# Optimization experiments

Measured on AMD Instinct MI355X. Metric: run time of the kernel, lower is better.

The kernel has to match this reference:

```python
import jax, jax.numpy as jnp
import numpy as np

ALPHA_SCALE = 9.9
EPS_LN = 1e-5
EPS_NORM = 1e-12


def _ln(x, g, b):
    m = x.mean(axis=-1, keepdims=True)
    v = ((x - m) ** 2).mean(axis=-1, keepdims=True)
    return (x - m) / jnp.sqrt(v + EPS_LN) * g + b


def setup_inputs() -> dict:
    key = jax.random.key(0)
    ks = jax.random.split(key, 8)
    B, D, U = 32, 4096, 64
    return {
        "stimulus": jax.random.normal(ks[0], (B, D), jnp.float32),
        "prev_act": jax.random.normal(ks[1], (B, D), jnp.float32),
        "W_heb": jax.random.normal(ks[2], (D, D), jnp.float32),
        "W_rec": jax.random.normal(ks[3], (D, D), jnp.float32),
        "decay": jax.random.uniform(ks[4], (D,), jnp.float32),
        "ln_rec_g": jnp.ones((D,), jnp.float32),
        "ln_rec_b": jnp.zeros((D,), jnp.float32),
        "fc1_w": jax.random.normal(ks[5], (D, 512), jnp.float32) * 0.02,
        "fc1_b": jnp.zeros((512,), jnp.float32),
        "ln1_g": jnp.ones((512,), jnp.float32),
        "ln1_b": jnp.zeros((512,), jnp.float32),
        "fc2_w": jax.random.normal(ks[6], (512, 256), jnp.float32) * 0.05,
        "fc2_b": jnp.zeros((256,), jnp.float32),
        "ln2_g": jnp.ones((256,), jnp.float32),
        "ln2_b": jnp.zeros((256,), jnp.float32),
        "fc3_w": jax.random.normal(ks[7], (256, U), jnp.float32) * 0.05,
        "fc3_b": jnp.zeros((U,), jnp.float32),
        "lno_g": jnp.ones((U,), jnp.float32),
        "lno_b": jnp.zeros((U,), jnp.float32),
    }


def reference(stimulus, prev_act, W_heb, W_rec, decay, ln_rec_g, ln_rec_b,
              fc1_w, fc1_b, ln1_g, ln1_b, fc2_w, fc2_b, ln2_g, ln2_b,
              fc3_w, fc3_b, lno_g, lno_b):
    D = W_heb.shape[0]
    U = fc3_b.shape[0]
    # recurrent path
    rec_out = jax.nn.relu(prev_act @ W_rec)           # [B, D]
    rec_norm = _ln(rec_out, ln_rec_g, ln_rec_b)
    # stimulus path
    stim_out = jax.nn.relu(stimulus @ W_heb)          # [B, D]
    final = stim_out + rec_norm                       # [B, D]
    # neuromodulator MLP -> dopamine (mean over batch)
    h = jax.nn.relu(_ln(final @ fc1_w + fc1_b, ln1_g, ln1_b))
    h = jax.nn.relu(_ln(h @ fc2_w + fc2_b, ln2_g, ln2_b))
    dop = jnp.tanh(_ln(h @ fc3_w + fc3_b, lno_g, lno_b)).mean(axis=0)  # [U]
    alpha = jnp.repeat(dop, D // U) * ALPHA_SCALE                      # [D]
    # Hebbian updates: batched outer products accumulated = GEMM
    heb_upd = jnp.einsum('bi,bj->ij', stimulus, stim_out)   # [D, D]
    rec_upd = jnp.einsum('bi,bj->ij', prev_act, rec_out)    # [D, D]
    W1 = W_heb + heb_upd * alpha[None, :]
    W2 = W_rec + rec_upd * alpha[None, :]
    # decay: W - diag(decay) @ W == (1 - decay) row-scale
    W1 = W1 * (1.0 - decay)[:, None]
    W2 = W2 * (1.0 - decay)[:, None]
    # row-wise L2 normalize (F.normalize p=2 dim=1)
    W1 = W1 / jnp.maximum(jnp.linalg.norm(W1, axis=1, keepdims=True), EPS_NORM)
    W2 = W2 / jnp.maximum(jnp.linalg.norm(W2, axis=1, keepdims=True), EPS_NORM)
    # [B+2D, D]: final_output followed by the two updated weight buffers
    return jnp.concatenate([final, W1, W2], axis=0)
```

## Files before the change

### kernel.cpp

```cpp
#include <hip/hip_runtime.h>
#include <stdint.h>

typedef unsigned short ushort_t;
typedef float f32x4 __attribute__((ext_vector_type(4)));
typedef short s16x8 __attribute__((ext_vector_type(8)));

#define B_  32
#define D_  4096
#define H1_ 512
#define H2_ 256
#define U_  64

#define KS_   16
#define KCH_  256
#define NT_   128
#define APAD  264
#define WPAD  70

__device__ __forceinline__ float bf2f(ushort_t u) {
    return __uint_as_float(((uint32_t)u) << 16);
}
__device__ __forceinline__ ushort_t f2bfu(float f) {
    uint32_t x = __float_as_uint(f);
    return (ushort_t)((x + 0x7fffu + ((x >> 16) & 1u)) >> 16);
}
__device__ __forceinline__ uint32_t pk2bf(float a, float b) {
    return ((uint32_t)f2bfu(a)) | (((uint32_t)f2bfu(b)) << 16);
}

__global__ __launch_bounds__(256, 4) void k_gemm_mfma(
    const float* __restrict__ stim, const float* __restrict__ prev,
    const float* __restrict__ Wheb, const float* __restrict__ Wrec,
    float* __restrict__ Psum, int ns)
{
    __shared__ ushort_t Al[32 * APAD];
    __shared__ ushort_t Wt[NT_ * WPAD];

    int bx = blockIdx.x;
    int gemm  = bx >> 9;
    int rem   = bx & 511;
    int nblk  = rem >> 4;
    int chunk = rem & 15;
    const float* A = gemm ? prev : stim;
    const float* W = gemm ? Wrec : Wheb;
    int k0c = chunk * KCH_;
    int n0  = nblk * NT_;
    int tid = threadIdx.x, lane = tid & 63, wave = tid >> 6;
    int col = lane & 15, quad = lane >> 4;

#pragma unroll
    for (int p = 0; p < 8; p++) {
        int idx = p * 256 + tid;
        int b   = idx >> 6;
        int k4  = (idx & 63) * 4;
        float4 v = *(const float4*)(A + (size_t)b * D_ + k0c + k4);
        uint2 w; w.x = pk2bf(v.x, v.y); w.y = pk2bf(v.z, v.w);
        *(uint2*)&Al[b * APAD + k4] = w;
    }

    f32x4 acc[2][2];
#pragma unroll
    for (int mt = 0; mt < 2; mt++)
#pragma unroll
        for (int nt = 0; nt < 2; nt++)
            acc[mt][nt] = (f32x4){0.f, 0.f, 0.f, 0.f};

    int m = tid & 31;
    int g = tid >> 5;

    for (int ks = 0; ks < 4; ks++) {
        __syncthreads();
        const float* Wb = W + (size_t)(k0c + ks * 64) * D_ + n0 + m * 4;
#pragma unroll
        for (int i = 0; i < 4; i++) {
            int kp = g + 8 * i;
            const float* p0 = Wb + (size_t)(2 * kp) * D_;
            float4 r0 = *(const float4*)p0;
            float4 r1 = *(const float4*)(p0 + D_);
            *(uint32_t*)&Wt[(m * 4 + 0) * WPAD + 2 * kp] = pk2bf(r0.x, r1.x);
            *(uint32_t*)&Wt[(m * 4 + 1) * WPAD + 2 * kp] = pk2bf(r0.y, r1.y);
            *(uint32_t*)&Wt[(m * 4 + 2) * WPAD + 2 * kp] = pk2bf(r0.z, r1.z);
            *(uint32_t*)&Wt[(m * 4 + 3) * WPAD + 2 * kp] = pk2bf(r0.w, r1.w);
        }
        __syncthreads();

#pragma unroll
        for (int kq = 0; kq < 2; kq++) {
            int kb = ks * 64 + kq * 32 + quad * 8;
            int kw = kq * 32 + quad * 8;
            s16x8 af[2], bf[2];
            af[0] = *(const s16x8*)&Al[col * APAD + kb];
            af[1] = *(const s16x8*)&Al[(col + 16) * APAD + kb];
#pragma unroll
            for (int nt = 0; nt < 2; nt++)
                bf[nt] = *(const s16x8*)&Wt[(wave * 32 + nt * 16 + col) * WPAD + kw];
#pragma unroll
            for (int mt = 0; mt < 2; mt++)
#pragma unroll
                for (int nt = 0; nt < 2; nt++)
                    acc[mt][nt] = __builtin_amdgcn_mfma_f32_16x16x32_bf16(
                        af[mt], bf[nt], acc[mt][nt], 0, 0, 0);
        }
    }

    int slice = chunk % ns;
    float* P = Psum + ((size_t)slice * 2 + gemm) * 32 * D_;
    if (ns == 16) {
#pragma unroll
        for (int mt = 0; mt < 2; mt++)
#pragma unroll
            for (int nt = 0; nt < 2; nt++)
#pragma unroll
                for (int r = 0; r < 4; r++) {
                    int b = mt * 16 + quad * 4 + r;
                    int n = n0 + wave * 32 + nt * 16 + col;
                    P[(size_t)b * D_ + n] = acc[mt][nt][r];
                }
    } else {
#pragma unroll
        for (int mt = 0; mt < 2; mt++)
#pragma unroll
            for (int nt = 0; nt < 2; nt++)
#pragma unroll
                for (int r = 0; r < 4; r++) {
                    int b = mt * 16 + quad * 4 + r;
                    int n = n0 + wave * 32 + nt * 16 + col;
                    atomicAdd(&P[(size_t)b * D_ + n], acc[mt][nt][r]);
                }
    }
}

__global__ __launch_bounds__(256) void k_reduce(
    const float* __restrict__ Psum,
    const float* __restrict__ stim, const float* __restrict__ prev,
    float* __restrict__ P_relu, ushort_t* __restrict__ Tbuf, int ns)
{
    int idx = blockIdx.x * 256 + threadIdx.x;
    int gemm = idx >> 17;
    int r    = idx & 131071;
    int b    = r >> 12;
    int d    = r & 4095;
    float s = 0.f;
    for (int sl = 0; sl < ns; sl++)
        s += Psum[((size_t)sl * 2 + gemm) * 131072 + r];
    s = fmaxf(s, 0.f);
    P_relu[idx] = s;
    Tbuf[(2 + gemm) * 131072 + d * 32 + b] = f2bfu(s);
    Tbuf[gemm * 131072 + d * 32 + b] = f2bfu((gemm ? prev : stim)[r]);
}

__global__ __launch_bounds__(256) void k_final_ln(
    const float* __restrict__ P_relu,
    const float* __restrict__ g, const float* __restrict__ be,
    float* __restrict__ dout, float* __restrict__ finalf32)
{
    __shared__ float red[256], red2[256];
    int b = blockIdx.x, tid = threadIdx.x;
    const float* rec = P_relu + 131072 + b * D_;
    const float* stm = P_relu + b * D_;

    float s = 0.f, s2 = 0.f;
    for (int d = tid; d < D_; d += 256) { float x = rec[d]; s += x; s2 += x * x; }
    red[tid] = s; red2[tid] = s2; __syncthreads();
    for (int st = 128; st > 0; st >>= 1) {
        if (tid < st) { red[tid] += red[tid + st]; red2[tid] += red2[tid + st]; }
        __syncthreads();
    }
    float m = red[0] * (1.f / D_);
    float v = red2[0] * (1.f / D_) - m * m;
    float rstd = rsqrtf(v + 1e-5f);

    for (int d = tid; d < D_; d += 256) {
        float fn = stm[d] + (rec[d] - m) * rstd * g[d] + be[d];
        finalf32[b * D_ + d] = fn;
        dout[b * D_ + d] = fn;
    }
}

__global__ __launch_bounds__(256) void k_fc1(
    const float* __restrict__ finalf32, const float* __restrict__ fc1w,
    float* __restrict__ z1p)
{
    int kc = blockIdx.x;
    int t  = threadIdx.x;
    int k0 = kc * 64;
    const float2* W2 = (const float2*)fc1w;

    float a0[32], a1[32];
#pragma unroll
    for (int b = 0; b < 32; b++) { a0[b] = 0.f; a1[b] = 0.f; }

    for (int k = k0; k < k0 + 64; k++) {
        float2 wv = W2[k * (H1_ / 2) + t];
#pragma unroll
        for (int b = 0; b < 32; b++) {
            float a = finalf32[b * D_ + k];
            a0[b] = fmaf(a, wv.x, a0[b]);
            a1[b] = fmaf(a, wv.y, a1[b]);
        }
    }
    float* P = z1p + (size_t)kc * 32 * H1_;
#pragma unroll
    for (int b = 0; b < 32; b++) {
        P[b * H1_ + 2 * t]     = a0[b];
        P[b * H1_ + 2 * t + 1] = a1[b];
    }
}

__global__ __launch_bounds__(256) void k_tail(
    const float* __restrict__ z1p,
    const float* __restrict__ fc1b,
    const float* __restrict__ ln1g, const float* __restrict__ ln1b,
    const float* __restrict__ fc2w, const float* __restrict__ fc2b,
    const float* __restrict__ ln2g, const float* __restrict__ ln2b,
    const float* __restrict__ fc3w, const float* __restrict__ fc3b,
    const float* __restrict__ lnog, const float* __restrict__ lnob,
    float* __restrict__ tanhout)
{
    __shared__ float sm[512];
    __shared__ float red[256], red2[256];
    __shared__ float h2s[256];
    int b = blockIdx.x, tid = threadIdx.x;

    for (int j = tid; j < H1_; j += 256) {
        float s = fc1b[j];
        for (int c = 0; c < 64; c++)
            s += z1p[((size_t)c * 32 + b) * H1_ + j];
        sm[j] = s;
    }
    __syncthreads();

    float s = 0.f, s2 = 0.f;
    for (int j = tid; j < H1_; j += 256) { float x = sm[j]; s += x; s2 += x * x; }
    red[tid] = s; red2[tid] = s2; __syncthreads();
    for (int st = 128; st > 0; st >>= 1) {
        if (tid < st) { red[tid] += red[tid + st]; red2[tid] += red2[tid + st]; }
        __syncthreads();
    }
    float m = red[0] * (1.f / H1_);
    float v = red2[0] * (1.f / H1_) - m * m;
    float rstd = rsqrtf(v + 1e-5f);
    __syncthreads();
    for (int j = tid; j < H1_; j += 256) {
        float h = (sm[j] - m) * rstd * ln1g[j] + ln1b[j];
        sm[j] = fmaxf(h, 0.f);
    }
    __syncthreads();

    float acc = fc2b[tid];
    for (int k = 0; k < H1_; k++)
        acc = fmaf(sm[k], fc2w[k * H2_ + tid], acc);
    red[tid] = acc; red2[tid] = acc * acc; __syncthreads();
    for (int st = 128; st > 0; st >>= 1) {
        if (tid < st) { red[tid] += red[tid + st]; red2[tid] += red2[tid + st]; }
        __syncthreads();
    }
    float m2 = red[0] * (1.f / H2_);
    float v2 = red2[0] * (1.f / H2_) - m2 * m2;
    float rstd2 = rsqrtf(v2 + 1e-5f);
    float h2 = fmaxf((acc - m2) * rstd2 * ln2g[tid] + ln2b[tid], 0.f);
    __syncthreads();
    h2s[tid] = h2; __syncthreads();

    int j  = tid & 63;
    int ks = tid >> 6;
    float p = 0.f;
    for (int kk = 0; kk < 64; kk++) {
        int k = ks * 64 + kk;
        p = fmaf(h2s[k], fc3w[k * U_ + j], p);
    }
    red[tid] = p; __syncthreads();
    if (tid < 64) {
        float x = red[tid] + red[tid + 64] + red[tid + 128] + red[tid + 192]
                + fc3b[tid];
        float ss = x, qq = x * x;
#pragma unroll
        for (int off = 32; off; off >>= 1) {
            ss += __shfl_xor(ss, off, 64);
            qq += __shfl_xor(qq, off, 64);
        }
        float m3 = ss * (1.f / U_);
        float v3 = qq * (1.f / U_) - m3 * m3;
        float to = tanhf((x - m3) * rsqrtf(v3 + 1e-5f) * lnog[tid] + lnob[tid]);
        tanhout[b * U_ + tid] = to;
    }
}

__global__ __launch_bounds__(512, 2) void k_update(
    const float* __restrict__ Wheb, const float* __restrict__ Wrec,
    const float* __restrict__ decay, const float* __restrict__ tanhout,
    const ushort_t* __restrict__ Tbuf, float* __restrict__ dout)
{
    __shared__ float ssl[8][16];
    int bx   = blockIdx.x;
    int mat  = bx >> 8;
    int i0   = (bx & 255) * 16;
    int tid  = threadIdx.x;
    int wave = tid >> 6, lane = tid & 63;
    int col  = lane & 15, quad = lane >> 4;

    float al = 0.f;
#pragma unroll
    for (int b = 0; b < 32; b++) al += tanhout[b * U_ + lane];
    al *= (9.9f / 32.f);

    const ushort_t* Sp = Tbuf + mat * 131072;
    const ushort_t* Op = Tbuf + (2 + mat) * 131072;
    const float*    Wp = mat ? Wrec : Wheb;

    s16x8 bfr = *(const s16x8*)&Sp[(i0 + col) * 32 + quad * 8];

    float dc = 1.f - decay[i0 + col];

    uint32_t vc[32][2];
    float ss = 0.f;

#pragma unroll
    for (int t = 0; t < 32; t++) {
        int tile = t * 8 + wave;
        int j0   = tile * 16;
        float av = __shfl(al, tile >> 2, 64);
        s16x8 af = *(const s16x8*)&Op[(j0 + col) * 32 + quad * 8];
        f32x4 u = (f32x4){0.f, 0.f, 0.f, 0.f};
        u = __builtin_amdgcn_mfma_f32_16x16x32_bf16(af, bfr, u, 0, 0, 0);
        const float4 w4 = *(const float4*)(Wp + (size_t)(i0 + col) * D_
                                           + j0 + quad * 4);
        float v0 = fmaf(av, u[0], w4.x) * dc;
        float v1 = fmaf(av, u[1], w4.y) * dc;
        float v2 = fmaf(av, u[2], w4.z) * dc;
        float v3 = fmaf(av, u[3], w4.w) * dc;
        ss = fmaf(v0, v0, ss);
        ss = fmaf(v1, v1, ss);
        ss = fmaf(v2, v2, ss);
        ss = fmaf(v3, v3, ss);
        vc[t][0] = pk2bf(v0, v1);
        vc[t][1] = pk2bf(v2, v3);
    }

    ss += __shfl_xor(ss, 16, 64);
    ss += __shfl_xor(ss, 32, 64);
    if (quad == 0) ssl[wave][col] = ss;
    __syncthreads();
    float st = 0.f;
#pragma unroll
    for (int w = 0; w < 8; w++) st += ssl[w][col];
    float ri = 1.f / fmaxf(sqrtf(st), 1e-12f);

    float* O = dout + (size_t)(32 + mat * D_ + i0 + col) * D_;
#pragma unroll
    for (int t = 0; t < 32; t++) {
        int j0 = (t * 8 + wave) * 16 + quad * 4;
        float4 o;
        o.x = __uint_as_float(vc[t][0] << 16)         * ri;
        o.y = __uint_as_float(vc[t][0] & 0xffff0000u) * ri;
        o.z = __uint_as_float(vc[t][1] << 16)         * ri;
        o.w = __uint_as_float(vc[t][1] & 0xffff0000u) * ri;
        *(float4*)(O + j0) = o;
    }
}

extern "C" void kernel_launch(void* const* d_in, const int* in_sizes, int n_in,
                              void* d_out, int out_size, void* d_ws, size_t ws_size,
                              hipStream_t stream)
{
    const float* stim = (const float*)d_in[0];
    const float* prev = (const float*)d_in[1];
    const float* Wheb = (const float*)d_in[2];
    const float* Wrec = (const float*)d_in[3];
    const float* decay= (const float*)d_in[4];
    const float* lnrg = (const float*)d_in[5];
    const float* lnrb = (const float*)d_in[6];
    const float* fc1w = (const float*)d_in[7];
    const float* fc1b = (const float*)d_in[8];
    const float* ln1g = (const float*)d_in[9];
    const float* ln1b = (const float*)d_in[10];
    const float* fc2w = (const float*)d_in[11];
    const float* fc2b = (const float*)d_in[12];
    const float* ln2g = (const float*)d_in[13];
    const float* ln2b = (const float*)d_in[14];
    const float* fc3w = (const float*)d_in[15];
    const float* fc3b = (const float*)d_in[16];
    const float* lnog = (const float*)d_in[17];
    const float* lnob = (const float*)d_in[18];

    const size_t FIXED = 1048576u + 1048576u + 524288u + 4194304u + 8192u;
    int ns = 16;
    if (ws_size < FIXED + 16u * 1048576u) {
        size_t avail = (ws_size > FIXED) ? (ws_size - FIXED) / 1048576u : 1u;
        ns = (int)avail;
        if (ns < 1) ns = 1;
        if (ns > 16) ns = 16;
    }

    char* ws = (char*)d_ws;
    float*    P_sum   = (float*)(ws + 0);
    char*     rest    = ws + (size_t)ns * 1048576u;
    float*    P_relu  = (float*)(rest + 0);
    ushort_t* P_tbuf  = (ushort_t*)(rest + 1048576);
    float*    P_final = (float*)(rest + 2097152);
    float*    P_z1p   = (float*)(rest + 2621440);
    float*    P_tanh  = (float*)(rest + 6815744);

    float* out = (float*)d_out;

    if (ns < 16)
        hipMemsetAsync(P_sum, 0, (size_t)ns * 1048576u, stream);

    k_gemm_mfma<<<1024, 256, 0, stream>>>(stim, prev, Wheb, Wrec, P_sum, ns);
    k_reduce   <<<1024, 256, 0, stream>>>(P_sum, stim, prev, P_relu, P_tbuf, ns);
    k_final_ln <<<32,   256, 0, stream>>>(P_relu, lnrg, lnrb, out, P_final);
    k_fc1      <<<64,   256, 0, stream>>>(P_final, fc1w, P_z1p);
    k_tail     <<<32,   256, 0, stream>>>(P_z1p, fc1b, ln1g, ln1b, fc2w, fc2b,
                                          ln2g, ln2b, fc3w, fc3b, lnog, lnob, P_tanh);
    k_update   <<<512,  512, 0, stream>>>(Wheb, Wrec, decay, P_tanh, P_tbuf, out);
}
```

Before: 403.2 us.

## Prefetch GEMM weight tiles, coalesce reduce transposes, vectorize LN, drop duplicate final buffer

The GEMM kernel now loads the next 64-row W chunk into registers while the current chunk is packed to LDS, so global load latency overlaps with the MFMA work. The reduce kernel processes float4 slices and transposes through shared memory, which turns the scattered 2-byte transposed writes into coalesced 8-byte writes. The final LayerNorm uses float4 loads and stores and no longer writes a separate fp32 copy; fc1 reads the output buffer directly. These changes cost extra registers in the GEMM and an LDS barrier in the reduce kernel.

```diff
diff --git a/kernel.cpp b/kernel.cpp
--- a/kernel.cpp
+++ b/kernel.cpp
@@ -68,19 +68,35 @@
     int m = tid & 31;
     int g = tid >> 5;
 
+    float4 pr0[4], pr1[4];
+    {
+        const float* Wb = W + (size_t)k0c * D_ + n0 + m * 4;
+#pragma unroll
+        for (int i = 0; i < 4; i++) {
+            int kp = g + 8 * i;
+            pr0[i] = *(const float4*)(Wb + (size_t)(2 * kp) * D_);
+            pr1[i] = *(const float4*)(Wb + (size_t)(2 * kp) * D_ + D_);
+        }
+    }
+
     for (int ks = 0; ks < 4; ks++) {
         __syncthreads();
-        const float* Wb = W + (size_t)(k0c + ks * 64) * D_ + n0 + m * 4;
 #pragma unroll
         for (int i = 0; i < 4; i++) {
             int kp = g + 8 * i;
-            const float* p0 = Wb + (size_t)(2 * kp) * D_;
-            float4 r0 = *(const float4*)p0;
-            float4 r1 = *(const float4*)(p0 + D_);
-            *(uint32_t*)&Wt[(m * 4 + 0) * WPAD + 2 * kp] = pk2bf(r0.x, r1.x);
-            *(uint32_t*)&Wt[(m * 4 + 1) * WPAD + 2 * kp] = pk2bf(r0.y, r1.y);
-            *(uint32_t*)&Wt[(m * 4 + 2) * WPAD + 2 * kp] = pk2bf(r0.z, r1.z);
-            *(uint32_t*)&Wt[(m * 4 + 3) * WPAD + 2 * kp] = pk2bf(r0.w, r1.w);
+            *(uint32_t*)&Wt[(m * 4 + 0) * WPAD + 2 * kp] = pk2bf(pr0[i].x, pr1[i].x);
+            *(uint32_t*)&Wt[(m * 4 + 1) * WPAD + 2 * kp] = pk2bf(pr0[i].y, pr1[i].y);
+            *(uint32_t*)&Wt[(m * 4 + 2) * WPAD + 2 * kp] = pk2bf(pr0[i].z, pr1[i].z);
+            *(uint32_t*)&Wt[(m * 4 + 3) * WPAD + 2 * kp] = pk2bf(pr0[i].w, pr1[i].w);
+        }
+        if (ks < 3) {
+            const float* Wb = W + (size_t)(k0c + (ks + 1) * 64) * D_ + n0 + m * 4;
+#pragma unroll
+            for (int i = 0; i < 4; i++) {
+                int kp = g + 8 * i;
+                pr0[i] = *(const float4*)(Wb + (size_t)(2 * kp) * D_);
+                pr1[i] = *(const float4*)(Wb + (size_t)(2 * kp) * D_ + D_);
+            }
         }
         __syncthreads();
 
@@ -135,24 +151,49 @@
     const float* __restrict__ stim, const float* __restrict__ prev,
     float* __restrict__ P_relu, ushort_t* __restrict__ Tbuf, int ns)
 {
-    int idx = blockIdx.x * 256 + threadIdx.x;
-    int gemm = idx >> 17;
-    int r    = idx & 131071;
-    int b    = r >> 12;
-    int d    = r & 4095;
-    float s = 0.f;
-    for (int sl = 0; sl < ns; sl++)
-        s += Psum[((size_t)sl * 2 + gemm) * 131072 + r];
-    s = fmaxf(s, 0.f);
-    P_relu[idx] = s;
-    Tbuf[(2 + gemm) * 131072 + d * 32 + b] = f2bfu(s);
-    Tbuf[gemm * 131072 + d * 32 + b] = f2bfu((gemm ? prev : stim)[r]);
+    __shared__ ushort_t T0[32][33];
+    __shared__ ushort_t T1[32][33];
+    int bx   = blockIdx.x;
+    int gemm = bx >> 7;
+    int d0   = (bx & 127) * 32;
+    int tid  = threadIdx.x;
+    int b    = tid >> 3;
+    int dq   = (tid & 7) * 4;
+    const float* In = gemm ? prev : stim;
+    size_t base = (size_t)b * D_ + d0 + dq;
+
+    float4 s = {0.f, 0.f, 0.f, 0.f};
+    for (int sl = 0; sl < ns; sl++) {
+        float4 p = *(const float4*)(Psum + ((size_t)(sl * 2 + gemm)) * 131072 + base);
+        s.x += p.x; s.y += p.y; s.z += p.z; s.w += p.w;
+    }
+    s.x = fmaxf(s.x, 0.f); s.y = fmaxf(s.y, 0.f);
+    s.z = fmaxf(s.z, 0.f); s.w = fmaxf(s.w, 0.f);
+    *(float4*)(P_relu + (size_t)gemm * 131072 + base) = s;
+
+    float4 iv = *(const float4*)(In + base);
+    T1[dq + 0][b] = f2bfu(s.x);  T1[dq + 1][b] = f2bfu(s.y);
+    T1[dq + 2][b] = f2bfu(s.z);  T1[dq + 3][b] = f2bfu(s.w);
+    T0[dq + 0][b] = f2bfu(iv.x); T0[dq + 1][b] = f2bfu(iv.y);
+    T0[dq + 2][b] = f2bfu(iv.z); T0[dq + 3][b] = f2bfu(iv.w);
+    __syncthreads();
+
+    int d  = tid >> 3;
+    int i4 = (tid & 7) * 4;
+    size_t toff = (size_t)(d0 + d) * 32 + i4;
+    uint2 w0, w1;
+    w0.x = ((uint32_t)T0[d][i4 + 0]) | (((uint32_t)T0[d][i4 + 1]) << 16);
+    w0.y = ((uint32_t)T0[d][i4 + 2]) | (((uint32_t)T0[d][i4 + 3]) << 16);
+    w1.x = ((uint32_t)T1[d][i4 + 0]) | (((uint32_t)T1[d][i4 + 1]) << 16);
+    w1.y = ((uint32_t)T1[d][i4 + 2]) | (((uint32_t)T1[d][i4 + 3]) << 16);
+    *(uint2*)(Tbuf + (size_t)gemm * 131072 + toff)       = w0;
+    *(uint2*)(Tbuf + (size_t)(2 + gemm) * 131072 + toff) = w1;
 }
 
 __global__ __launch_bounds__(256) void k_final_ln(
     const float* __restrict__ P_relu,
     const float* __restrict__ g, const float* __restrict__ be,
-    float* __restrict__ dout, float* __restrict__ finalf32)
+    float* __restrict__ dout)
 {
     __shared__ float red[256], red2[256];
     int b = blockIdx.x, tid = threadIdx.x;
@@ -160,7 +201,11 @@
     const float* stm = P_relu + b * D_;
 
     float s = 0.f, s2 = 0.f;
-    for (int d = tid; d < D_; d += 256) { float x = rec[d]; s += x; s2 += x * x; }
+    for (int d = tid * 4; d < D_; d += 1024) {
+        float4 x = *(const float4*)(rec + d);
+        s  += x.x + x.y + x.z + x.w;
+        s2 += x.x * x.x + x.y * x.y + x.z * x.z + x.w * x.w;
+    }
     red[tid] = s; red2[tid] = s2; __syncthreads();
     for (int st = 128; st > 0; st >>= 1) {
         if (tid < st) { red[tid] += red[tid + st]; red2[tid] += red2[tid + st]; }
@@ -170,10 +215,17 @@
     float v = red2[0] * (1.f / D_) - m * m;
     float rstd = rsqrtf(v + 1e-5f);
 
-    for (int d = tid; d < D_; d += 256) {
-        float fn = stm[d] + (rec[d] - m) * rstd * g[d] + be[d];
-        finalf32[b * D_ + d] = fn;
-        dout[b * D_ + d] = fn;
+    for (int d = tid * 4; d < D_; d += 1024) {
+        float4 rv = *(const float4*)(rec + d);
+        float4 sv = *(const float4*)(stm + d);
+        float4 gv = *(const float4*)(g + d);
+        float4 bv = *(const float4*)(be + d);
+        float4 o;
+        o.x = sv.x + (rv.x - m) * rstd * gv.x + bv.x;
+        o.y = sv.y + (rv.y - m) * rstd * gv.y + bv.y;
+        o.z = sv.z + (rv.z - m) * rstd * gv.z + bv.z;
+        o.w = sv.w + (rv.w - m) * rstd * gv.w + bv.w;
+        *(float4*)(dout + (size_t)b * D_ + d) = o;
     }
 }
 
@@ -397,7 +449,6 @@
     char*     rest    = ws + (size_t)ns * 1048576u;
     float*    P_relu  = (float*)(rest + 0);
     ushort_t* P_tbuf  = (ushort_t*)(rest + 1048576);
-    float*    P_final = (float*)(rest + 2097152);
     float*    P_z1p   = (float*)(rest + 2621440);
     float*    P_tanh  = (float*)(rest + 6815744);
 
@@ -407,9 +458,9 @@
         hipMemsetAsync(P_sum, 0, (size_t)ns * 1048576u, stream);
 
     k_gemm_mfma<<<1024, 256, 0, stream>>>(stim, prev, Wheb, Wrec, P_sum, ns);
-    k_reduce   <<<1024, 256, 0, stream>>>(P_sum, stim, prev, P_relu, P_tbuf, ns);
-    k_final_ln <<<32,   256, 0, stream>>>(P_relu, lnrg, lnrb, out, P_final);
-    k_fc1      <<<64,   256, 0, stream>>>(P_final, fc1w, P_z1p);
+    k_reduce   <<<256,  256, 0, stream>>>(P_sum, stim, prev, P_relu, P_tbuf, ns);
+    k_final_ln <<<32,   256, 0, stream>>>(P_relu, lnrg, lnrb, out);
+    k_fc1      <<<64,   256, 0, stream>>>(out, fc1w, P_z1p);
     k_tail     <<<32,   256, 0, stream>>>(P_z1p, fc1b, ln1g, ln1b, fc2w, fc2b,
                                           ln2g, ln2b, fc3w, fc3b, lnog, lnob, P_tanh);
     k_update   <<<512,  512, 0, stream>>>(Wheb, Wrec, decay, P_tanh, P_tbuf, out);
```

Result: no change. 401.3 us (-0.5%).
